# Kernel optimization log

Measured on AMD Instinct MI355X. Metric: run time of the kernel, lower is better.

The kernel has to match this reference:

```python
import jax, jax.numpy as jnp
from jax import lax
import numpy as np

KS = 15          # dark-channel window
PAD = (KS - 1) // 2
TEMP = 10000.0   # positional encoding temperature
NPF = 32         # max(num_pos_feats_x, y, z)
EPS = 1e-6


def _conv1x1(x, w, b):
    # x: [B,C,H,W], w: [O,C], b: [O]
    return jnp.einsum('bchw,oc->bohw', x, w) + b[None, :, None, None]


def _conv2s2(x, w, b):
    # kernel 2, stride 2, no padding; w: [O,I,2,2]
    y = lax.conv_general_dilated(x, w, (2, 2), 'VALID',
                                 dimension_numbers=('NCHW', 'OIHW', 'NCHW'))
    return y + b[None, :, None, None]


def _lrelu(x):
    return jnp.where(x >= 0, x, 0.1 * x)


def _resize(x, h, w):
    return jax.image.resize(x, (x.shape[0], x.shape[1], h, w), method='bilinear')


def _dark_channel(x):
    # min over channels, reflect pad, 15x15 sliding min (== unfold+min in torch)
    dm = jnp.min(x, axis=1, keepdims=True)  # [B,1,H,W]
    dm = jnp.pad(dm, ((0, 0), (0, 0), (PAD, PAD), (PAD, PAD)), mode='reflect')
    return lax.reduce_window(dm, jnp.inf, lax.min,
                             (1, 1, KS, KS), (1, 1, 1, 1), 'VALID')


def _sincos(e, d, dim_t):
    # e: [B,H,W] -> [B,H,W,d] with interleaved sin/cos (torch stack+flatten)
    p = e[..., None] / dim_t[:d]
    return jnp.stack((jnp.sin(p[..., 0::2]), jnp.cos(p[..., 1::2])),
                     axis=4).reshape(e.shape + (d,))


def _pos_encoding(x, dark):
    B, _, H, W = x.shape
    scale = 2.0 * np.pi
    yv = jnp.arange(H, dtype=jnp.float32)
    xv = jnp.arange(W, dtype=jnp.float32)
    ye = jnp.broadcast_to((yv / (yv[-1] + EPS) * scale)[None, :, None], (B, H, W))
    xe = jnp.broadcast_to((xv / (xv[-1] + EPS) * scale)[None, None, :], (B, H, W))
    z = dark[:, 0]
    ze = z / (jnp.max(z, axis=(1, 2), keepdims=True) + EPS) * scale
    dim_t = TEMP ** (2.0 * (jnp.arange(NPF, dtype=jnp.float32) // 2) / NPF)
    pos_x = _sincos(xe, 16, dim_t)
    pos_y = _sincos(ye, 16, dim_t)
    pos_z = _sincos(ze, 32, dim_t)
    return jnp.concatenate((pos_x, pos_y, pos_z), axis=3).transpose(0, 3, 1, 2)


def _forward(x, w_cf1, b_cf1, w_e1, b_e1, w_e2, b_e2, w_d1, b_d1, w_d2, b_d2,
             w_pha1, b_pha1, w_pha2, b_pha2, w_amp1, b_amp1, w_amp2, b_amp2,
             w_spat1, b_spat1, w_spat2, b_spat2, w_u1, b_u1, w_u2, b_u2,
             w_u3, b_u3, w_u4, b_u4, w_cf2, b_cf2, w_cf3, b_cf3):
    xori = x
    dark = _dark_channel(1.0 - x)            # DCP of inverted image [B,1,512,512]
    ape = _pos_encoding(x, dark) + _conv1x1(x, w_cf1, b_cf1)  # [B,64,H,W]

    x_f = _conv1x1(_conv1x1(x, w_e1, b_e1), w_e2, b_e2)       # [B,64,512,512]
    x_d1 = _conv2s2(x_f, w_d1, b_d1)                          # [B,128,256,256]
    x_d2 = _conv2s2(x_d1, w_d2, b_d2)                         # [B,256,128,128]
    Hd, Wd = x_d2.shape[2], x_d2.shape[3]

    x_freq = jnp.fft.rfft2(x_d2)             # norm='backward' (default)
    x_pha = jnp.angle(x_freq)
    x_amp = jnp.abs(x_freq)
    # phase branch is computed but unused downstream (matches original code)
    x_pha = _conv1x1(_lrelu(_conv1x1(x_pha, w_pha1, b_pha1)), w_pha2, b_pha2)
    x_amp = _conv1x1(_lrelu(_conv1x1(x_amp, w_amp1, b_amp1)), w_amp2, b_amp2)
    x_four = jnp.fft.irfft2(lax.complex(x_amp * jnp.cos(x_amp),
                                        x_amp * jnp.sin(x_amp)), s=(Hd, Wd))
    x_four = _conv1x1(_resize(x_four, x_d1.shape[2], x_d1.shape[3]), w_u1, b_u1)
    x_four = _conv1x1(_resize(x_four, x_f.shape[2], x_f.shape[3]), w_u2, b_u2)

    x_spat = _conv1x1(_lrelu(_conv1x1(x_d2, w_spat1, b_spat1)), w_spat2, b_spat2)
    x_spat = _conv1x1(_resize(x_spat, x_d1.shape[2], x_d1.shape[3]), w_u3, b_u3)
    x_spat = _conv1x1(_resize(x_spat, x_f.shape[2], x_f.shape[3]), w_u4, b_u4)
    x_spat = x_spat * ape

    four_spa = jnp.concatenate((x_four, x_spat), axis=1)      # [B,128,512,512]
    out = _conv1x1(_conv1x1(four_spa, w_cf2, b_cf2), w_cf3, b_cf3)
    return out + xori


def setup_inputs() -> dict:
    key = jax.random.key(0)
    ks = iter(jax.random.split(key, 64))
    def W(*shape):
        return 0.02 * jax.random.normal(next(ks), shape, dtype=jnp.float32)
    def Bb(n):
        return 0.01 * jax.random.normal(next(ks), (n,), dtype=jnp.float32)
    nc = 64
    inp = {'x': jax.random.uniform(next(ks), (1, 3, 512, 512), dtype=jnp.float32)}
    inp.update(w_cf1=W(nc, 3), b_cf1=Bb(nc))
    inp.update(w_e1=W(nc // 8, 3), b_e1=Bb(nc // 8))
    inp.update(w_e2=W(nc, nc // 8), b_e2=Bb(nc))
    inp.update(w_d1=W(2 * nc, nc, 2, 2), b_d1=Bb(2 * nc))
    inp.update(w_d2=W(4 * nc, 2 * nc, 2, 2), b_d2=Bb(4 * nc))
    for nm in ('pha', 'amp', 'spat'):
        inp['w_%s1' % nm] = W(4 * nc, 4 * nc); inp['b_%s1' % nm] = Bb(4 * nc)
        inp['w_%s2' % nm] = W(4 * nc, 4 * nc); inp['b_%s2' % nm] = Bb(4 * nc)
    inp.update(w_u1=W(2 * nc, 4 * nc), b_u1=Bb(2 * nc))
    inp.update(w_u2=W(nc, 2 * nc), b_u2=Bb(nc))
    inp.update(w_u3=W(2 * nc, 4 * nc), b_u3=Bb(2 * nc))
    inp.update(w_u4=W(nc, 2 * nc), b_u4=Bb(nc))
    inp.update(w_cf2=W(nc, 2 * nc), b_cf2=Bb(nc))
    inp.update(w_cf3=W(3, nc), b_cf3=Bb(3))
    return inp


def reference(x, w_cf1, b_cf1, w_e1, b_e1, w_e2, b_e2, w_d1, b_d1, w_d2, b_d2,
              w_pha1, b_pha1, w_pha2, b_pha2, w_amp1, b_amp1, w_amp2, b_amp2,
              w_spat1, b_spat1, w_spat2, b_spat2, w_u1, b_u1, w_u2, b_u2,
              w_u3, b_u3, w_u4, b_u4, w_cf2, b_cf2, w_cf3, b_cf3):
    return _forward(x, w_cf1, b_cf1, w_e1, b_e1, w_e2, b_e2, w_d1, b_d1,
                    w_d2, b_d2, w_pha1, b_pha1, w_pha2, b_pha2, w_amp1, b_amp1,
                    w_amp2, b_amp2, w_spat1, b_spat1, w_spat2, b_spat2,
                    w_u1, b_u1, w_u2, b_u2, w_u3, b_u3, w_u4, b_u4,
                    w_cf2, b_cf2, w_cf3, b_cf3)
```

## Files before the change

### kernel.cpp

```cpp
#include <hip/hip_runtime.h>
#include <math.h>

#define PI_F 3.14159265358979323846f
#define NPIX 262144

typedef __attribute__((ext_vector_type(8))) short sh8;
typedef __attribute__((ext_vector_type(4))) float fx4;
typedef __attribute__((ext_vector_type(4))) unsigned short ush4;

__device__ __forceinline__ unsigned short f2bf(float v) {
    unsigned u = __float_as_uint(v);
    return (unsigned short)((u + 0x7FFFu + ((u >> 16) & 1)) >> 16);
}
__device__ __forceinline__ float bf2f(unsigned short h) {
    return __uint_as_float((unsigned)h << 16);
}

__device__ __forceinline__ int refl512(int t) {
    if (t < 0) t = -t;
    if (t > 511) t = 1022 - t;
    return t;
}

__global__ __launch_bounds__(256) void k_mrow(const float* __restrict__ x, float* __restrict__ tmp,
                                              int* __restrict__ gmax) {
    __shared__ float row[512];
    int i = blockIdx.x, tid = threadIdx.x;
    if (i == 0 && tid == 0) gmax[0] = 0;
    #pragma unroll
    for (int h = 0; h < 2; h++) {
        int j = tid + h * 256;
        int p = (i << 9) + j;
        float m = fmaxf(x[p], fmaxf(x[p + NPIX], x[p + 2 * NPIX]));
        row[j] = 1.0f - m;
    }
    __syncthreads();
    #pragma unroll
    for (int h = 0; h < 2; h++) {
        int j = tid + h * 256;
        float m = 1e30f;
        #pragma unroll
        for (int d = -7; d <= 7; d++) m = fminf(m, row[refl512(j + d)]);
        tmp[(i << 9) + j] = m;
    }
}

__global__ __launch_bounds__(256) void k_mincol_max(const float* __restrict__ tmp, float* __restrict__ dark,
                                                    int* __restrict__ gmax) {
    int p = blockIdx.x * 256 + threadIdx.x;
    int i = p >> 9, j = p & 511;
    float m = 1e30f;
    #pragma unroll
    for (int d = -7; d <= 7; d++) m = fminf(m, tmp[(refl512(i + d) << 9) + j]);
    dark[p] = m;
    __shared__ float red[256];
    int tid = threadIdx.x;
    red[tid] = m;
    __syncthreads();
    for (int s = 128; s > 0; s >>= 1) {
        if (tid < s) red[tid] = fmaxf(red[tid], red[tid + s]);
        __syncthreads();
    }
    if (tid == 0) atomicMax(gmax, __float_as_int(red[0]));
}

__device__ __forceinline__ void prep_one(const float* __restrict__ w, unsigned short* __restrict__ h,
                                         unsigned short* __restrict__ l, int N, int K, int cshift, int idx) {
    if (idx >= N * K) return;
    int n = idx / K, kord = idx - n * K;
    int ksrc = kord;
    if (cshift) {
        int dydx = kord >> cshift, c = kord & ((1 << cshift) - 1);
        ksrc = c * 4 + dydx;
    }
    float v = w[n * K + ksrc];
    unsigned short hb = f2bf(v);
    h[idx] = hb;
    if (l) l[idx] = f2bf(v - bf2f(hb));
}

__global__ __launch_bounds__(256) void k_prepA(
    const float* __restrict__ w_d2, unsigned short* __restrict__ d2h, unsigned short* __restrict__ d2l,
    const float* __restrict__ w_a1, unsigned short* __restrict__ a1h, unsigned short* __restrict__ a1l,
    const float* __restrict__ w_a2, unsigned short* __restrict__ a2h, unsigned short* __restrict__ a2l,
    const float* __restrict__ w_s1, unsigned short* __restrict__ s1h,
    unsigned short* __restrict__ BfH, unsigned short* __restrict__ BfL,
    unsigned short* __restrict__ BfcH, unsigned short* __restrict__ BfcL,
    unsigned short* __restrict__ BicH, unsigned short* __restrict__ BicL,
    unsigned short* __restrict__ BirH, unsigned short* __restrict__ BirL,
    float* __restrict__ zbias) {
    int b = blockIdx.x, tid = threadIdx.x;
    if (b < 512)       { prep_one(w_d2, d2h, d2l, 256, 512, 7, b * 256 + tid); return; }
    else if (b < 768)  { prep_one(w_a1, a1h, a1l, 256, 256, 0, (b - 512) * 256 + tid); return; }
    else if (b < 1024) { prep_one(w_a2, a2h, a2l, 256, 256, 0, (b - 768) * 256 + tid); return; }
    else if (b < 1280) { prep_one(w_s1, s1h, nullptr, 256, 256, 0, (b - 1024) * 256 + tid); return; }
    int idx = (b - 1280) * 256 + tid;
    if (idx < 256) zbias[idx] = 0.f;
    const float w0 = 2.f * PI_F / 128.f;
    float v;
    unsigned short *H, *L;
    int off;
    if (idx < 32768) {
        int n = idx >> 7, k = idx & 127;
        int t = n & 127, r = (t * k) & 127;
        float s_, c_; sincosf(w0 * r, &s_, &c_);
        v = (n < 128) ? c_ : -s_;
        H = BfH; L = BfL; off = idx;
    } else if (idx < 98304) {
        int i = idx - 32768;
        int n = i >> 8, j = i & 255;
        int t = n & 127, r = (t * (j & 127)) & 127;
        float s_, c_; sincosf(w0 * r, &s_, &c_);
        v = (n < 128) ? ((j < 128) ? c_ : s_) : ((j < 128) ? -s_ : c_);
        H = BfcH; L = BfcL; off = i;
    } else if (idx < 163840) {
        int i = idx - 98304;
        int n = i >> 8, j = i & 255;
        int t = n & 127, r = (t * (j & 127)) & 127;
        float s_, c_; sincosf(w0 * r, &s_, &c_);
        v = ((n < 128) ? ((j < 128) ? c_ : -s_) : ((j < 128) ? s_ : c_)) * (1.f / 128.f);
        H = BicH; L = BicL; off = i;
    } else if (idx < 184320) {
        int i = idx - 163840;
        int col = i / 160, j = i - col * 160;
        if (j == 0) v = 1.f / 128.f;
        else if (j < 64)  { int r = (j * col) & 127; float s_, c_; sincosf(w0 * r, &s_, &c_); v = 2.f * c_ / 128.f; }
        else if (j == 64) v = (col & 1) ? -1.f / 128.f : 1.f / 128.f;
        else if (j >= 66 && j <= 128) { int k = j - 65; int r = (k * col) & 127; float s_, c_; sincosf(w0 * r, &s_, &c_); v = -2.f * s_ / 128.f; }
        else v = 0.f;
        H = BirH; L = BirL; off = i;
    } else return;
    unsigned short hb = f2bf(v);
    H[off] = hb;
    L[off] = f2bf(v - bf2f(hb));
}

__global__ __launch_bounds__(256) void k_prepB(
    const float* __restrict__ w_u3, const float* __restrict__ w_u4, float* __restrict__ Uf,
    const float* __restrict__ w_e1, const float* __restrict__ b_e1,
    const float* __restrict__ w_e2, const float* __restrict__ b_e2,
    const float* __restrict__ w_d1, const float* __restrict__ b_d1,
    unsigned short* __restrict__ d1ch, float* __restrict__ b1c,
    const float* __restrict__ b_u3, const float* __restrict__ b_u4, float* __restrict__ b43,
    const float* __restrict__ w2, const float* __restrict__ b2,
    const float* __restrict__ w3, const float* __restrict__ b3,
    const float* __restrict__ wu2, const float* __restrict__ bu2,
    const float* __restrict__ wu1, const float* __restrict__ bu1,
    float* __restrict__ Wc, float* __restrict__ bc,
    float* __restrict__ W21c, float* __restrict__ b21c) {
    int b = blockIdx.x, tid = threadIdx.x;
    if (b < 64) {
        int idx = b * 256 + tid;
        int n = idx >> 8, j = idx & 255;
        float s = 0.f;
        #pragma unroll 16
        for (int o = 0; o < 128; o++) s += w_u4[n * 128 + o] * w_u3[o * 256 + j];
        Uf[idx] = s;
    } else if (b < 80) {
        __shared__ float E[192];
        if (tid < 192) {
            int o = tid / 3, ci = tid - o * 3;
            float s = 0.f;
            #pragma unroll
            for (int r = 0; r < 8; r++) s += w_e2[o * 8 + r] * w_e1[r * 3 + ci];
            E[tid] = s;
        }
        __syncthreads();
        int idx = (b - 64) * 256 + tid;
        int n = idx >> 5, k = idx & 31;
        float s = 0.f;
        if (k < 12) {
            int dydx = k / 3, ci = k - dydx * 3;
            #pragma unroll 16
            for (int o = 0; o < 64; o++) s += w_d1[n * 256 + o * 4 + dydx] * E[o * 3 + ci];
        }
        d1ch[idx] = f2bf(s);
    } else if (b == 80) {
        __shared__ float f[64];
        if (tid < 64) {
            int o = tid;
            float s = b_e2[o];
            #pragma unroll
            for (int r = 0; r < 8; r++) s += w_e2[o * 8 + r] * b_e1[r];
            f[o] = s;
        }
        __syncthreads();
        if (tid < 128) {
            float s = b_d1[tid];
            #pragma unroll 8
            for (int o = 0; o < 64; o++) {
                float fo = f[o];
                #pragma unroll
                for (int dydx = 0; dydx < 4; dydx++) s += w_d1[tid * 256 + o * 4 + dydx] * fo;
            }
            b1c[tid] = s;
        }
    } else if (b == 81) {
        if (tid < 64) {
            float s = b_u4[tid];
            #pragma unroll 16
            for (int o = 0; o < 128; o++) s += w_u4[tid * 128 + o] * b_u3[o];
            b43[tid] = s;
        }
    } else {
        __shared__ float sWc[384], sW2c[384];
        if (tid < 128) {
            int j = tid;
            for (int r = 0; r < 3; r++) {
                float s = 0.f;
                #pragma unroll 16
                for (int o = 0; o < 64; o++) s += w3[r * 64 + o] * w2[o * 128 + j];
                sWc[r * 128 + j] = s;
                Wc[r * 128 + j] = s;
            }
            if (j < 3) {
                float s = b3[j];
                #pragma unroll 16
                for (int o = 0; o < 64; o++) s += w3[j * 64 + o] * b2[o];
                bc[j] = s;
            }
        }
        __syncthreads();
        if (tid < 128) {
            int j = tid;
            for (int r = 0; r < 3; r++) {
                float s = 0.f;
                #pragma unroll 16
                for (int o = 0; o < 64; o++) s += sWc[r * 128 + o] * wu2[o * 128 + j];
                sW2c[r * 128 + j] = s;
            }
        }
        __syncthreads();
        if (tid < 256) {
            int j = tid;
            for (int r = 0; r < 3; r++) {
                float s = 0.f;
                #pragma unroll 16
                for (int o = 0; o < 128; o++) s += sW2c[r * 128 + o] * wu1[o * 256 + j];
                W21c[r * 256 + j] = s;
            }
        }
        if (tid < 3) {
            float s = 0.f;
            #pragma unroll 16
            for (int o = 0; o < 128; o++) s += sW2c[tid * 128 + o] * bu1[o];
            #pragma unroll 16
            for (int o = 0; o < 64; o++)  s += sWc[tid * 128 + o] * bu2[o];
            b21c[tid] = s;
        }
    }
}

__global__ __launch_bounds__(256) void k_prep2(const float* __restrict__ Uf, const float* __restrict__ wsp2,
                                               const float* __restrict__ bsp2, const float* __restrict__ b43,
                                               unsigned short* __restrict__ Wg, float* __restrict__ bgc) {
    __shared__ float u[256], red[256];
    int n = blockIdx.x, tid = threadIdx.x;
    u[tid] = Uf[n * 256 + tid];
    __syncthreads();
    float s = 0.f;
    #pragma unroll 16
    for (int o = 0; o < 256; o++) s += u[o] * wsp2[o * 256 + tid];
    Wg[n * 256 + tid] = f2bf(s);
    red[tid] = u[tid] * bsp2[tid];
    __syncthreads();
    for (int st = 128; st > 0; st >>= 1) {
        if (tid < st) red[tid] += red[tid + st];
        __syncthreads();
    }
    if (tid == 0) bgc[n] = b43[n] + red[0];
}

template<int AMODE, int SPLIT, int LRELU, int TSTORE, int ABF16, int CBF16>
__global__ __launch_bounds__(256) void k_mmcf(const void* __restrict__ Asrc_,
                                              const unsigned short* __restrict__ Bh,
                                              const unsigned short* __restrict__ Bl,
                                              const float* __restrict__ bias, void* __restrict__ C_,
                                              int M, int N, int K, int cshift, int wshift, int srcW,
                                              int gy) {
    const float* Af = (const float*)Asrc_;
    const unsigned short* A16 = (const unsigned short*)Asrc_;
    float* Cf = (float*)C_;
    unsigned short* C16 = (unsigned short*)C_;
    __shared__ unsigned short AhS[128 * 40];
    __shared__ unsigned short BhS[64 * 40];
    __shared__ unsigned short AlS[SPLIT ? 128 * 40 : 8];
    __shared__ unsigned short BlS[SPLIT ? 64 * 40 : 8];
    int tid = threadIdx.x;
    int nwg = (int)gridDim.x;
    int bid = blockIdx.x;
    int qq = nwg >> 3, rr = nwg & 7;
    int xcd = bid & 7, ixw = bid >> 3;
    int work = (xcd < rr) ? (xcd * (qq + 1) + ixw) : (rr * (qq + 1) + (xcd - rr) * qq + ixw);
    int bx = work / gy;
    int by = work - bx * gy;
    int m0 = bx * 128;
    int n0 = by * 64;
    int wave = tid >> 6, lane = tid & 63;
    int wm = (wave >> 1) * 64, wn = (wave & 1) * 32;
    int l15 = lane & 15, quad = lane >> 4;
    int lk = quad * 8, lk4 = quad * 4;
    fx4 acc[4][2];
    #pragma unroll
    for (int a = 0; a < 4; a++)
        #pragma unroll
        for (int b = 0; b < 2; b++)
            acc[a][b] = (fx4){0.f, 0.f, 0.f, 0.f};

    int mm = tid & 127;
    int kpb = tid >> 7;
    int gm = m0 + mm;
    int oj = 0, oi = 0, cA = 0, kfA = 0, tauA = 0;
    size_t abase = 0;
    if (AMODE == 1) { oj = gm & ((1 << wshift) - 1); oi = gm >> wshift; }
    if (AMODE == 2) { oj = gm & 255; oi = gm >> 8; }
    if (AMODE == 3) abase = (size_t)gm * K;
    if (AMODE == 7) { cA = gm / 65; kfA = gm - cA * 65; }
    if (AMODE == 8) { cA = gm >> 7; tauA = gm & 127; }
    if (AMODE == 9) { cA = gm / 65; kfA = gm - cA * 65; }

    for (int kb = 0; kb < K; kb += 32) {
        if (AMODE == 3 && ABF16 && !SPLIT) {
            #pragma unroll
            for (int half = 0; half < 2; half++) {
                sh8 hv = *(const sh8*)(const void*)&A16[abase + kb + kpb * 16 + half * 8];
                *(sh8*)(void*)&AhS[mm * 40 + (kpb * 2 + half) * 8] = hv;
            }
        } else {
            #pragma unroll
            for (int half = 0; half < 2; half++) {
                sh8 hv, lv;
                #pragma unroll
                for (int tt = 0; tt < 4; tt++) {
                    int kp = kpb * 8 + half * 4 + tt;
                    int k0 = kb + kp * 2;
                    unsigned short h0, h1;
                    if (ABF16) {
                        size_t ad0, ad1;
                        if (AMODE == 0) {
                            ad0 = (size_t)k0 * M + gm;
                            ad1 = ad0 + M;
                        } else if (AMODE == 1) {
                            int c = k0 & ((1 << cshift) - 1);
                            int dydx = k0 >> cshift;
                            int dy = dydx >> 1, dx = dydx & 1;
                            size_t pix = (size_t)(2 * oi + dy) * srcW + (2 * oj + dx);
                            size_t plane = (size_t)srcW * srcW;
                            ad0 = (size_t)c * plane + pix;
                            ad1 = ad0 + plane;
                        } else if (AMODE == 3) {
                            ad0 = abase + k0;
                            ad1 = ad0 + 1;
                        } else if (AMODE == 7) {
                            int t0 = k0 & 127, hf = k0 >> 7;
                            ad0 = (size_t)(cA * 128 + t0) * 256 + hf * 128 + kfA;
                            ad1 = ad0 + 256;
                        } else {
                            int j0 = k0, j1 = k0 + 1;
                            int kf0 = (j0 < 65) ? j0 : ((j0 < 130) ? j0 - 65 : 0);
                            int hf0 = (j0 >= 65 && j0 < 130) ? 1 : 0;
                            int kf1 = (j1 < 65) ? j1 : ((j1 < 130) ? j1 - 65 : 0);
                            int hf1 = (j1 >= 65 && j1 < 130) ? 1 : 0;
                            ad0 = (size_t)(cA * 65 + kf0) * 256 + hf0 * 128 + tauA;
                            ad1 = (size_t)(cA * 65 + kf1) * 256 + hf1 * 128 + tauA;
                        }
                        h0 = A16[ad0];
                        h1 = A16[ad1];
                    } else {
                        float a0, a1;
                        if (AMODE == 2) {
                            if (k0 < 12) {
                                int d0 = k0 / 3, c0 = k0 - d0 * 3;
                                int k1 = k0 + 1;
                                int d1x = k1 / 3, c1 = k1 - d1x * 3;
                                a0 = Af[(size_t)c0 * NPIX + (size_t)(2 * oi + (d0 >> 1)) * 512 + 2 * oj + (d0 & 1)];
                                a1 = Af[(size_t)c1 * NPIX + (size_t)(2 * oi + (d1x >> 1)) * 512 + 2 * oj + (d1x & 1)];
                            } else { a0 = 0.f; a1 = 0.f; }
                        } else if (AMODE == 9) {
                            size_t ad = (size_t)cA * 16640 + (size_t)k0 * 65 + kfA;
                            float re0 = Af[ad], im0 = Af[ad + 2129920];
                            float re1 = Af[ad + 65], im1 = Af[ad + 65 + 2129920];
                            a0 = sqrtf(re0 * re0 + im0 * im0);
                            a1 = sqrtf(re1 * re1 + im1 * im1);
                        } else {
                            size_t ad0 = (size_t)k0 * M + gm;
                            a0 = Af[ad0];
                            a1 = Af[ad0 + M];
                        }
                        h0 = f2bf(a0);
                        h1 = f2bf(a1);
                        if (SPLIT) {
                            lv[tt * 2] = (short)f2bf(a0 - bf2f(h0));
                            lv[tt * 2 + 1] = (short)f2bf(a1 - bf2f(h1));
                        }
                    }
                    hv[tt * 2] = (short)h0;
                    hv[tt * 2 + 1] = (short)h1;
                }
                int coff = (kpb * 2 + half) * 8;
                *(sh8*)(void*)&AhS[mm * 40 + coff] = hv;
                if (SPLIT) *(sh8*)(void*)&AlS[mm * 40 + coff] = lv;
            }
        }
        {
            int n = tid >> 2, seg = tid & 3;
            size_t gb = (size_t)(n0 + n) * K + kb + seg * 8;
            *(sh8*)(void*)&BhS[n * 40 + seg * 8] = *(const sh8*)(const void*)&Bh[gb];
            if (SPLIT) *(sh8*)(void*)&BlS[n * 40 + seg * 8] = *(const sh8*)(const void*)&Bl[gb];
        }
        __syncthreads();
        sh8 af[4], bf[2], afl[4], bfl[2];
        #pragma unroll
        for (int mt = 0; mt < 4; mt++) {
            af[mt] = *(const sh8*)(const void*)&AhS[(wm + mt * 16 + l15) * 40 + lk];
            if (SPLIT) afl[mt] = *(const sh8*)(const void*)&AlS[(wm + mt * 16 + l15) * 40 + lk];
        }
        #pragma unroll
        for (int nt = 0; nt < 2; nt++) {
            bf[nt] = *(const sh8*)(const void*)&BhS[(wn + nt * 16 + l15) * 40 + lk];
            if (SPLIT) bfl[nt] = *(const sh8*)(const void*)&BlS[(wn + nt * 16 + l15) * 40 + lk];
        }
        #pragma unroll
        for (int mt = 0; mt < 4; mt++)
            #pragma unroll
            for (int nt = 0; nt < 2; nt++) {
                acc[mt][nt] = __builtin_amdgcn_mfma_f32_16x16x32_bf16(af[mt], bf[nt], acc[mt][nt], 0, 0, 0);
                if (SPLIT) {
                    acc[mt][nt] = __builtin_amdgcn_mfma_f32_16x16x32_bf16(af[mt], bfl[nt], acc[mt][nt], 0, 0, 0);
                    acc[mt][nt] = __builtin_amdgcn_mfma_f32_16x16x32_bf16(afl[mt], bf[nt], acc[mt][nt], 0, 0, 0);
                }
            }
        __syncthreads();
    }
    #pragma unroll
    for (int nt = 0; nt < 2; nt++) {
        int n = n0 + wn + nt * 16 + l15;
        float bs = bias[n];
        #pragma unroll
        for (int mt = 0; mt < 4; mt++) {
            int mbase = m0 + wm + mt * 16 + lk4;
            if (TSTORE) {
                #pragma unroll
                for (int r = 0; r < 4; r++) {
                    float q = acc[mt][nt][r] + bs;
                    if (LRELU) q = (q < 0.f) ? 0.1f * q : q;
                    if (CBF16) C16[(size_t)(mbase + r) * N + n] = f2bf(q);
                    else       Cf[(size_t)(mbase + r) * N + n] = q;
                }
            } else if (CBF16) {
                ush4 v;
                #pragma unroll
                for (int r = 0; r < 4; r++) {
                    float q = acc[mt][nt][r] + bs;
                    if (LRELU) q = (q < 0.f) ? 0.1f * q : q;
                    v[r] = f2bf(q);
                }
                *(ush4*)(void*)&C16[(size_t)n * M + mbase] = v;
            } else {
                float4 v;
                float* vp = (float*)&v;
                #pragma unroll
                for (int r = 0; r < 4; r++) {
                    float q = acc[mt][nt][r] + bs;
                    if (LRELU) q = (q < 0.f) ? 0.1f * q : q;
                    vp[r] = q;
                }
                *(float4*)&Cf[(size_t)n * M + mbase] = v;
            }
        }
    }
}

__global__ __launch_bounds__(256) void k_zbuild(const float* __restrict__ A2, unsigned short* __restrict__ Z) {
    int idx = blockIdx.x * 256 + threadIdx.x;
    int ct = idx / 65, kf = idx - ct * 65;
    int c = ct >> 7, t = ct & 127;
    float a = A2[idx];
    float s_, c_;
    sincosf(a, &s_, &c_);
    size_t m = (size_t)c * 65 + kf;
    Z[(size_t)t * 16640 + m] = f2bf(a * c_);
    Z[2129920 + (size_t)t * 16640 + m] = f2bf(a * s_);
}

__global__ __launch_bounds__(64) void k_h3s(const float* __restrict__ I2T, const float* __restrict__ W21c,
                                            const float* __restrict__ b21c, float* __restrict__ h3s) {
    __shared__ float wa[768], bs[3];
    int tid = threadIdx.x;
    for (int i = tid; i < 768; i += 64) wa[i] = W21c[i];
    if (tid < 3) bs[tid] = b21c[tid];
    __syncthreads();
    int q = blockIdx.x * 64 + tid;
    float a0 = bs[0], a1 = bs[1], a2 = bs[2];
    #pragma unroll 4
    for (int c = 0; c < 256; c++) {
        float v = I2T[(size_t)c * 16384 + q];
        a0 += wa[c] * v;
        a1 += wa[256 + c] * v;
        a2 += wa[512 + c] * v;
    }
    h3s[q] = a0; h3s[16384 + q] = a1; h3s[32768 + q] = a2;
}

__global__ __launch_bounds__(256) void k_final(const float* __restrict__ x,
                                               const float* __restrict__ dark, const int* __restrict__ gmax,
                                               const float* __restrict__ wcf1, const float* __restrict__ bcf1,
                                               const float* __restrict__ Wc, const float* __restrict__ bc,
                                               const float* __restrict__ g4s, const float* __restrict__ h3s,
                                               float* __restrict__ out) {
    __shared__ float dimt[32], w1[192], b1[64], wb[192], bcs[3];
    int tid = threadIdx.x;
    if (tid < 32) dimt[tid] = powf(10000.f, (float)(2 * (tid >> 1)) / 32.f);
    if (tid < 192) w1[tid] = wcf1[tid];
    if (tid < 64) b1[tid] = bcf1[tid];
    if (tid < 192) { int r = tid / 64, c = tid - (tid / 64) * 64; wb[tid] = Wc[r * 128 + 64 + c]; }
    if (tid < 3) bcs[tid] = bc[tid];
    __syncthreads();
    int p = blockIdx.x * 256 + threadIdx.x;
    int i = p >> 9, j = p & 511;
    const float scale = 2.f * PI_F;
    float inv511 = scale / (511.f + 1e-6f);
    float xe = (float)j * inv511, ye = (float)i * inv511;
    float gm = __int_as_float(gmax[0]);
    float ze = dark[p] / (gm + 1e-6f) * scale;
    float x0 = x[p], x1 = x[p + NPIX], x2 = x[p + 2 * NPIX];

    int ky = i >> 2, ry = i & 3;
    int ym = (ky > 0) ? ky - 1 : 0, yp = (ky < 127) ? ky + 1 : 127;
    float wy0 = (ry == 0) ? .375f : (ry == 1) ? .1875f : (ry == 2) ? .0625f : 0.f;
    float wy1 = (ry == 0 || ry == 3) ? .625f : .75f;
    float wy2 = (ry == 0) ? 0.f : (ry == 1) ? .0625f : (ry == 2) ? .1875f : .375f;
    int kx = j >> 2, rx = j & 3;
    int xm = (kx > 0) ? kx - 1 : 0, xp = (kx < 127) ? kx + 1 : 127;
    float wx0 = (rx == 0) ? .375f : (rx == 1) ? .1875f : (rx == 2) ? .0625f : 0.f;
    float wx1 = (rx == 0 || rx == 3) ? .625f : .75f;
    float wx2 = (rx == 0) ? 0.f : (rx == 1) ? .0625f : (rx == 2) ? .1875f : .375f;
    int r0 = ym * 128, r1 = ky * 128, r2 = yp * 128;
    int o00 = r0 + xm, o01 = r0 + kx, o02 = r0 + xp;
    int o10 = r1 + xm, o11 = r1 + kx, o12 = r1 + xp;
    int o20 = r2 + xm, o21 = r2 + kx, o22 = r2 + xp;

    float a0 = 0.f, a1 = 0.f, a2 = 0.f;
    #pragma unroll 1
    for (int c = 0; c < 64; c++) {
        float e = (c < 16) ? xe / dimt[c] : (c < 32) ? ye / dimt[c - 16] : ze / dimt[c - 32];
        float sn, cs;
        __sincosf(e, &sn, &cs);
        float pos = ((c & 1) == 0) ? sn : cs;
        float ape = pos + w1[c * 3] * x0 + w1[c * 3 + 1] * x1 + w1[c * 3 + 2] * x2 + b1[c];
        const float* gp = g4s + (size_t)c * 16384;
        float gv = wy0 * (wx0 * gp[o00] + wx1 * gp[o01] + wx2 * gp[o02])
                 + wy1 * (wx0 * gp[o10] + wx1 * gp[o11] + wx2 * gp[o12])
                 + wy2 * (wx0 * gp[o20] + wx1 * gp[o21] + wx2 * gp[o22]);
        float s = gv * ape;
        a0 += wb[c] * s; a1 += wb[64 + c] * s; a2 += wb[128 + c] * s;
    }
    float f0, f1, f2;
    {
        const float* hp = h3s;
        f0 = wy0 * (wx0 * hp[o00] + wx1 * hp[o01] + wx2 * hp[o02])
           + wy1 * (wx0 * hp[o10] + wx1 * hp[o11] + wx2 * hp[o12])
           + wy2 * (wx0 * hp[o20] + wx1 * hp[o21] + wx2 * hp[o22]);
        hp = h3s + 16384;
        f1 = wy0 * (wx0 * hp[o00] + wx1 * hp[o01] + wx2 * hp[o02])
           + wy1 * (wx0 * hp[o10] + wx1 * hp[o11] + wx2 * hp[o12])
           + wy2 * (wx0 * hp[o20] + wx1 * hp[o21] + wx2 * hp[o22]);
        hp = h3s + 32768;
        f2 = wy0 * (wx0 * hp[o00] + wx1 * hp[o01] + wx2 * hp[o02])
           + wy1 * (wx0 * hp[o10] + wx1 * hp[o11] + wx2 * hp[o12])
           + wy2 * (wx0 * hp[o20] + wx1 * hp[o21] + wx2 * hp[o22]);
    }
    out[p]            = a0 + f0 + bcs[0] + x0;
    out[NPIX + p]     = a1 + f1 + bcs[1] + x1;
    out[2 * NPIX + p] = a2 + f2 + bcs[2] + x2;
}

extern "C" void kernel_launch(void* const* d_in, const int* in_sizes, int n_in,
                              void* d_out, int out_size, void* d_ws, size_t ws_size,
                              hipStream_t stream) {
    const float* x      = (const float*)d_in[0];
    const float* w_cf1  = (const float*)d_in[1];  const float* b_cf1 = (const float*)d_in[2];
    const float* w_e1   = (const float*)d_in[3];  const float* b_e1  = (const float*)d_in[4];
    const float* w_e2   = (const float*)d_in[5];  const float* b_e2  = (const float*)d_in[6];
    const float* w_d1   = (const float*)d_in[7];  const float* b_d1  = (const float*)d_in[8];
    const float* w_d2   = (const float*)d_in[9];  const float* b_d2  = (const float*)d_in[10];
    const float* w_amp1 = (const float*)d_in[15]; const float* b_amp1 = (const float*)d_in[16];
    const float* w_amp2 = (const float*)d_in[17]; const float* b_amp2 = (const float*)d_in[18];
    const float* w_sp1  = (const float*)d_in[19]; const float* b_sp1  = (const float*)d_in[20];
    const float* w_sp2  = (const float*)d_in[21]; const float* b_sp2  = (const float*)d_in[22];
    const float* w_u1   = (const float*)d_in[23]; const float* b_u1   = (const float*)d_in[24];
    const float* w_u2   = (const float*)d_in[25]; const float* b_u2   = (const float*)d_in[26];
    const float* w_u3   = (const float*)d_in[27]; const float* b_u3   = (const float*)d_in[28];
    const float* w_u4   = (const float*)d_in[29]; const float* b_u4   = (const float*)d_in[30];
    const float* w_cf2  = (const float*)d_in[31]; const float* b_cf2  = (const float*)d_in[32];
    const float* w_cf3  = (const float*)d_in[33]; const float* b_cf3  = (const float*)d_in[34];
    float* out = (float*)d_out;

    char* ws = (char*)d_ws;
    constexpr size_t MiB = 1ull << 20;
    float*  dark   = (float*)(ws + 0 * MiB);
    float*  tmp    = (float*)(ws + 1 * MiB);
    int*    gmax   = (int*)  (ws + 2 * MiB);
    float*  Wc     = (float*)(ws + 2 * MiB + 1024);
    float*  bc     = (float*)(ws + 2 * MiB + 2560);
    float*  W21c   = (float*)(ws + 2 * MiB + 4096);
    float*  b21c   = (float*)(ws + 2 * MiB + 7168);
    float*  b43    = (float*)(ws + 2 * MiB + 7424);
    unsigned short* d1ch = (unsigned short*)(ws + 3 * MiB);
    float*  b1c    = (float*)(ws + 3 * MiB + 16384);
    float*  Uf     = (float*)(ws + 3 * MiB + 32768);
    unsigned short* Wg = (unsigned short*)(ws + 3 * MiB + 131072);
    float*  bgc    = (float*)(ws + 3 * MiB + 196608);
    unsigned short* xd1 = (unsigned short*)(ws + 67 * MiB);
    unsigned short* xd2 = (unsigned short*)(ws + 99 * MiB);
    unsigned short* F1T = (unsigned short*)(ws + 115 * MiB);
    float*  F2C    = (float*)(ws + 147 * MiB);
    float*  A1     = (float*)(ws + 173 * MiB);
    float*  A2     = (float*)(ws + 182 * MiB);
    unsigned short* Zbuf = (unsigned short*)(ws + 115 * MiB);
    unsigned short* I1T  = (unsigned short*)(ws + 132 * MiB);
    float*  I2T    = (float*)(ws + 149 * MiB);
    float*  h3s    = (float*)(ws + 11 * MiB);
    unsigned short* s1 = (unsigned short*)(ws + 31 * MiB);
    float*  g4s    = (float*)(ws + 87 * MiB);
    unsigned short* wb16 = (unsigned short*)(ws + 192 * MiB);
    unsigned short* d2h = wb16 + 65536,   * d2l = wb16 + 196608;
    unsigned short* a1h = wb16 + 327680,  * a1l = wb16 + 393216;
    unsigned short* a2h = wb16 + 458752,  * a2l = wb16 + 524288;
    unsigned short* s1h = wb16 + 589824;
    unsigned short* BfH = wb16 + 786432,  * BfL = wb16 + 819200;
    unsigned short* BfcH = wb16 + 851968, * BfcL = wb16 + 917504;
    unsigned short* BicH = wb16 + 983040, * BicL = wb16 + 1048576;
    unsigned short* BirH = wb16 + 1114112,* BirL = wb16 + 1134592;
    float* zbias = (float*)(ws + 195 * MiB + 512 * 1024);

    k_mrow<<<512, 256, 0, stream>>>(x, tmp, gmax);
    k_mincol_max<<<1024, 256, 0, stream>>>(tmp, dark, gmax);
    k_prepA<<<2000, 256, 0, stream>>>(w_d2, d2h, d2l, w_amp1, a1h, a1l, w_amp2, a2h, a2l, w_sp1, s1h,
                                      BfH, BfL, BfcH, BfcL, BicH, BicL, BirH, BirL, zbias);
    k_prepB<<<83, 256, 0, stream>>>(w_u3, w_u4, Uf,
                                    w_e1, b_e1, w_e2, b_e2, w_d1, b_d1, d1ch, b1c,
                                    b_u3, b_u4, b43,
                                    w_cf2, b_cf2, w_cf3, b_cf3, w_u2, b_u2, w_u1, b_u1,
                                    Wc, bc, W21c, b21c);
    k_prep2<<<64, 256, 0, stream>>>(Uf, w_sp2, b_sp2, b43, Wg, bgc);

    k_mmcf<2, 0, 0, 0, 0, 1><<<1024, 256, 0, stream>>>(x, d1ch, nullptr, b1c, xd1, 65536, 128, 32, 0, 0, 0, 2);
    k_mmcf<1, 0, 0, 0, 1, 1><<<512, 256, 0, stream>>>(xd1, d2h, nullptr, b_d2, xd2, 16384, 256, 512, 7, 7, 256, 4);

    k_mmcf<3, 0, 0, 1, 1, 1><<<1024, 256, 0, stream>>>(xd2, BfH, nullptr, zbias, F1T, 32768, 256, 128, 0, 0, 0, 4);
    k_mmcf<7, 0, 0, 0, 1, 0><<<520, 256, 0, stream>>>(F1T, BfcH, nullptr, zbias, F2C, 16640, 256, 256, 0, 0, 0, 4);
    k_mmcf<9, 1, 1, 0, 0, 0><<<260, 256, 0, stream>>>(F2C, a1h, a1l, b_amp1, A1, 8320, 256, 256, 0, 0, 0, 4);
    k_mmcf<0, 1, 0, 0, 0, 0><<<260, 256, 0, stream>>>(A1, a2h, a2l, b_amp2, A2, 8320, 256, 256, 0, 0, 0, 4);
    k_zbuild<<<8320, 256, 0, stream>>>(A2, Zbuf);
    k_mmcf<0, 0, 0, 1, 1, 1><<<520, 256, 0, stream>>>(Zbuf, BicH, nullptr, zbias, I1T, 16640, 256, 256, 0, 0, 0, 4);
    k_mmcf<8, 0, 0, 1, 1, 0><<<512, 256, 0, stream>>>(I1T, BirH, nullptr, zbias, I2T, 32768, 128, 160, 0, 0, 0, 2);

    k_h3s<<<256, 64, 0, stream>>>(I2T, W21c, b21c, h3s);

    k_mmcf<0, 0, 1, 0, 1, 1><<<512, 256, 0, stream>>>(xd2, s1h, nullptr, b_sp1, s1, 16384, 256, 256, 0, 0, 0, 4);
    k_mmcf<0, 0, 0, 0, 1, 0><<<128, 256, 0, stream>>>(s1, Wg, nullptr, bgc, g4s, 16384, 64, 256, 0, 0, 0, 1);

    k_final<<<1024, 256, 0, stream>>>(x, dark, gmax, w_cf1, b_cf1, Wc, bc, g4s, h3s, out);
}
```

Before: 374.5 us.

## Stage vertically interpolated upsample rows in LDS for final fused kernel

Each block of the final kernel now covers half an image row. It first does the vertical bilinear pass of the 64-channel g4s map and the 3-channel h3s map into shared memory, so each pixel only needs three LDS reads per channel instead of nine scattered global loads. It also precomputes the row-constant y positional encodings once per block and replaces the per-channel divides by multiplies with reciprocals. The cost is about 18 KB of LDS per block, which may limit occupancy, plus an extra barrier and a staging phase.

```diff
diff --git a/kernel.cpp b/kernel.cpp
--- a/kernel.cpp
+++ b/kernel.cpp
@@ -508,68 +508,81 @@
                                                const float* __restrict__ Wc, const float* __restrict__ bc,
                                                const float* __restrict__ g4s, const float* __restrict__ h3s,
                                                float* __restrict__ out) {
-    __shared__ float dimt[32], w1[192], b1[64], wb[192], bcs[3];
+    __shared__ float idimt[32], w1[192], b1[64], wb[192], bcs[3], posy[16];
+    __shared__ float gyr[64][68];
+    __shared__ float hyr[3][68];
     int tid = threadIdx.x;
-    if (tid < 32) dimt[tid] = powf(10000.f, (float)(2 * (tid >> 1)) / 32.f);
+    int bid = blockIdx.x;
+    int i = bid >> 1;
+    int j0 = (bid & 1) << 8;
+    int j = j0 + tid;
+    int p = (i << 9) + j;
+
+    const float scale = 2.f * PI_F;
+    float inv511 = scale / (511.f + 1e-6f);
+    float ye = (float)i * inv511;
+
+    if (tid < 32) idimt[tid] = 1.f / powf(10000.f, (float)(2 * (tid >> 1)) / 32.f);
     if (tid < 192) w1[tid] = wcf1[tid];
     if (tid < 64) b1[tid] = bcf1[tid];
     if (tid < 192) { int r = tid / 64, c = tid - (tid / 64) * 64; wb[tid] = Wc[r * 128 + 64 + c]; }
     if (tid < 3) bcs[tid] = bc[tid];
     __syncthreads();
-    int p = blockIdx.x * 256 + threadIdx.x;
-    int i = p >> 9, j = p & 511;
-    const float scale = 2.f * PI_F;
-    float inv511 = scale / (511.f + 1e-6f);
-    float xe = (float)j * inv511, ye = (float)i * inv511;
-    float gm = __int_as_float(gmax[0]);
-    float ze = dark[p] / (gm + 1e-6f) * scale;
-    float x0 = x[p], x1 = x[p + NPIX], x2 = x[p + 2 * NPIX];
+    if (tid >= 32 && tid < 48) {
+        int c = tid - 32;
+        float e = ye * idimt[c];
+        posy[c] = ((c & 1) == 0) ? __sinf(e) : __cosf(e);
+    }
 
     int ky = i >> 2, ry = i & 3;
     int ym = (ky > 0) ? ky - 1 : 0, yp = (ky < 127) ? ky + 1 : 127;
     float wy0 = (ry == 0) ? .375f : (ry == 1) ? .1875f : (ry == 2) ? .0625f : 0.f;
     float wy1 = (ry == 0 || ry == 3) ? .625f : .75f;
     float wy2 = (ry == 0) ? 0.f : (ry == 1) ? .0625f : (ry == 2) ? .1875f : .375f;
-    int kx = j >> 2, rx = j & 3;
-    int xm = (kx > 0) ? kx - 1 : 0, xp = (kx < 127) ? kx + 1 : 127;
+    int base = j0 >> 2;
+    int r0 = ym * 128, r1 = ky * 128, r2 = yp * 128;
+    for (int idx = tid; idx < 64 * 66; idx += 256) {
+        int c = idx / 66, t = idx - c * 66;
+        int col = base - 1 + t;
+        col = (col < 0) ? 0 : (col > 127) ? 127 : col;
+        const float* gp = g4s + (size_t)c * 16384;
+        gyr[c][t] = wy0 * gp[r0 + col] + wy1 * gp[r1 + col] + wy2 * gp[r2 + col];
+    }
+    for (int idx = tid; idx < 3 * 66; idx += 256) {
+        int c = idx / 66, t = idx - c * 66;
+        int col = base - 1 + t;
+        col = (col < 0) ? 0 : (col > 127) ? 127 : col;
+        const float* hp = h3s + (size_t)c * 16384;
+        hyr[c][t] = wy0 * hp[r0 + col] + wy1 * hp[r1 + col] + wy2 * hp[r2 + col];
+    }
+    __syncthreads();
+
+    float xe = (float)j * inv511;
+    float gm = __int_as_float(gmax[0]);
+    float ze = dark[p] / (gm + 1e-6f) * scale;
+    float x0 = x[p], x1 = x[p + NPIX], x2 = x[p + 2 * NPIX];
+
+    int rx = j & 3;
+    int tx = tid >> 2;
     float wx0 = (rx == 0) ? .375f : (rx == 1) ? .1875f : (rx == 2) ? .0625f : 0.f;
     float wx1 = (rx == 0 || rx == 3) ? .625f : .75f;
     float wx2 = (rx == 0) ? 0.f : (rx == 1) ? .0625f : (rx == 2) ? .1875f : .375f;
-    int r0 = ym * 128, r1 = ky * 128, r2 = yp * 128;
-    int o00 = r0 + xm, o01 = r0 + kx, o02 = r0 + xp;
-    int o10 = r1 + xm, o11 = r1 + kx, o12 = r1 + xp;
-    int o20 = r2 + xm, o21 = r2 + kx, o22 = r2 + xp;
 
     float a0 = 0.f, a1 = 0.f, a2 = 0.f;
     #pragma unroll 1
     for (int c = 0; c < 64; c++) {
-        float e = (c < 16) ? xe / dimt[c] : (c < 32) ? ye / dimt[c - 16] : ze / dimt[c - 32];
-        float sn, cs;
-        __sincosf(e, &sn, &cs);
-        float pos = ((c & 1) == 0) ? sn : cs;
+        float pos;
+        if (c < 16)      { float e = xe * idimt[c];      pos = ((c & 1) == 0) ? __sinf(e) : __cosf(e); }
+        else if (c < 32) { pos = posy[c - 16]; }
+        else             { float e = ze * idimt[c - 32]; pos = ((c & 1) == 0) ? __sinf(e) : __cosf(e); }
         float ape = pos + w1[c * 3] * x0 + w1[c * 3 + 1] * x1 + w1[c * 3 + 2] * x2 + b1[c];
-        const float* gp = g4s + (size_t)c * 16384;
-        float gv = wy0 * (wx0 * gp[o00] + wx1 * gp[o01] + wx2 * gp[o02])
-                 + wy1 * (wx0 * gp[o10] + wx1 * gp[o11] + wx2 * gp[o12])
-                 + wy2 * (wx0 * gp[o20] + wx1 * gp[o21] + wx2 * gp[o22]);
+        float gv = wx0 * gyr[c][tx] + wx1 * gyr[c][tx + 1] + wx2 * gyr[c][tx + 2];
         float s = gv * ape;
         a0 += wb[c] * s; a1 += wb[64 + c] * s; a2 += wb[128 + c] * s;
     }
-    float f0, f1, f2;
-    {
-        const float* hp = h3s;
-        f0 = wy0 * (wx0 * hp[o00] + wx1 * hp[o01] + wx2 * hp[o02])
-           + wy1 * (wx0 * hp[o10] + wx1 * hp[o11] + wx2 * hp[o12])
-           + wy2 * (wx0 * hp[o20] + wx1 * hp[o21] + wx2 * hp[o22]);
-        hp = h3s + 16384;
-        f1 = wy0 * (wx0 * hp[o00] + wx1 * hp[o01] + wx2 * hp[o02])
-           + wy1 * (wx0 * hp[o10] + wx1 * hp[o11] + wx2 * hp[o12])
-           + wy2 * (wx0 * hp[o20] + wx1 * hp[o21] + wx2 * hp[o22]);
-        hp = h3s + 32768;
-        f2 = wy0 * (wx0 * hp[o00] + wx1 * hp[o01] + wx2 * hp[o02])
-           + wy1 * (wx0 * hp[o10] + wx1 * hp[o11] + wx2 * hp[o12])
-           + wy2 * (wx0 * hp[o20] + wx1 * hp[o21] + wx2 * hp[o22]);
-    }
+    float f0 = wx0 * hyr[0][tx] + wx1 * hyr[0][tx + 1] + wx2 * hyr[0][tx + 2];
+    float f1 = wx0 * hyr[1][tx] + wx1 * hyr[1][tx + 1] + wx2 * hyr[1][tx + 2];
+    float f2 = wx0 * hyr[2][tx] + wx1 * hyr[2][tx + 1] + wx2 * hyr[2][tx + 2];
     out[p]            = a0 + f0 + bcs[0] + x0;
     out[NPIX + p]     = a1 + f1 + bcs[1] + x1;
     out[2 * NPIX + p] = a2 + f2 + bcs[2] + x2;
```

Result: faster. 356.8 us (-4.7%).
